# Performance work log

Hardware: AMD Instinct MI355X
Metric: run time of the kernel (lower is better)

The kernel has to match this reference:

```python
import jax, jax.numpy as jnp
import numpy as np
import math

B, S, HID = 4, 2048, 1024
NH, HD = 16, 64  # num heads, head dim
ROPE_THETA = 10000.0


def rotate_half(x):
    x1, x2 = jnp.split(x, 2, axis=-1)
    return jnp.concatenate((-x2, x1), axis=-1)


def setup_inputs() -> dict:
    key = jax.random.key(0)
    ks = jax.random.split(key, 7)
    hidden_states = jax.random.normal(ks[0], (B, S, HID), dtype=jnp.float32)
    attention_mask = jnp.zeros((B, 1, S, S), dtype=jnp.float32)
    position_ids = jnp.sort(jax.random.randint(ks[1], (B, S), 0, S), axis=-1)
    scale = 1.0 / math.sqrt(HID)
    Wq = jax.random.normal(ks[2], (HID, HID), dtype=jnp.float32) * scale
    Wk = jax.random.normal(ks[3], (HID, HID), dtype=jnp.float32) * scale
    Wv = jax.random.normal(ks[4], (HID, HID), dtype=jnp.float32) * scale
    Wo = jax.random.normal(ks[5], (HID, HID), dtype=jnp.float32) * scale
    return {"hidden_states": hidden_states, "attention_mask": attention_mask,
            "position_ids": position_ids, "Wq": Wq, "Wk": Wk, "Wv": Wv, "Wo": Wo}


def reference(hidden_states, attention_mask, position_ids, Wq, Wk, Wv, Wo):
    dtype = hidden_states.dtype
    # QKV projections (torch Linear: x @ W.T), reshape to [B, H, S, D]
    def proj(W):
        return (hidden_states @ W.T).reshape(B, S, NH, HD).transpose(0, 2, 1, 3)
    q, k, v = proj(Wq), proj(Wk), proj(Wv)

    # Rotary embeddings: cos/sin cache of shape [S, HD], gathered by position_ids
    inv_freq = 1.0 / (ROPE_THETA ** (jnp.arange(0, HD, 2, dtype=jnp.float32) / HD))
    t = jnp.arange(S, dtype=jnp.float32)
    freqs = t[:, None] * inv_freq[None, :]            # [S, HD/2]
    emb = jnp.concatenate((freqs, freqs), axis=-1)     # [S, HD]
    cos = jnp.cos(emb).astype(dtype)[position_ids][:, None]  # [B, 1, S, HD]
    sin = jnp.sin(emb).astype(dtype)[position_ids][:, None]

    q = q * cos + rotate_half(q) * sin
    k = k * cos + rotate_half(k) * sin

    # Manual attention: scores, additive mask, fp32 softmax, weighted sum
    scores = jnp.einsum('bhqd,bhkd->bhqk', q, k) / math.sqrt(HD)
    scores = scores + attention_mask
    attn = jax.nn.softmax(scores.astype(jnp.float32), axis=-1).astype(dtype)
    out = jnp.einsum('bhqk,bhkd->bhqd', attn, v)       # [B, H, S, D]
    out = out.transpose(0, 2, 1, 3).reshape(B, S, HID)
    return out @ Wo.T
```

## Files before the change

### kernel.cpp

```cpp
#include <hip/hip_runtime.h>
#include <hip/hip_bf16.h>
#include <math.h>

typedef __bf16 bf16;
typedef bf16 bf16x4 __attribute__((ext_vector_type(4)));
typedef bf16 bf16x8 __attribute__((ext_vector_type(8)));
typedef float f32x4 __attribute__((ext_vector_type(4)));

#define B_ 4
#define S_ 2048
#define HID_ 1024
#define NH_ 16
#define HD_ 64
#define LTS 72

__device__ __forceinline__ void async16(const bf16* g, bf16* l) {
  __builtin_amdgcn_global_load_lds(
      (const __attribute__((address_space(1))) void*)g,
      (__attribute__((address_space(3))) void*)l, 16, 0, 0);
}

#define MM16(A, B, C) C = __builtin_amdgcn_mfma_f32_16x16x32_bf16(A, B, C, 0, 0, 0)

__global__ void cvt_kernel(const float* __restrict__ src, bf16* __restrict__ dst, int n4) {
  int i = blockIdx.x * 256 + threadIdx.x;
  if (i < n4) {
    float4 v = ((const float4*)src)[i];
    bf16x4 o;
    o[0] = (bf16)v.x; o[1] = (bf16)v.y; o[2] = (bf16)v.z; o[3] = (bf16)v.w;
    ((bf16x4*)dst)[i] = o;
  }
}

#define DECL_ACC \
  f32x4 a00 = {}, a01 = {}, a02 = {}, a03 = {}; \
  f32x4 a10 = {}, a11 = {}, a12 = {}, a13 = {}; \
  f32x4 a20 = {}, a21 = {}, a22 = {}, a23 = {}; \
  f32x4 a30 = {}, a31 = {}, a32 = {}, a33 = {};

#define KLOOP_FRAGS_MFMA \
    bf16x8 af0 = *(const bf16x8*)(lA + (wm + 0 * 16 + l16) * 32 + quad * 8); \
    bf16x8 af1 = *(const bf16x8*)(lA + (wm + 1 * 16 + l16) * 32 + quad * 8); \
    bf16x8 af2 = *(const bf16x8*)(lA + (wm + 2 * 16 + l16) * 32 + quad * 8); \
    bf16x8 af3 = *(const bf16x8*)(lA + (wm + 3 * 16 + l16) * 32 + quad * 8); \
    bf16x8 bg0 = *(const bf16x8*)(lB + (wn + 0 * 16 + l16) * 32 + quad * 8); \
    bf16x8 bg1 = *(const bf16x8*)(lB + (wn + 1 * 16 + l16) * 32 + quad * 8); \
    bf16x8 bg2 = *(const bf16x8*)(lB + (wn + 2 * 16 + l16) * 32 + quad * 8); \
    bf16x8 bg3 = *(const bf16x8*)(lB + (wn + 3 * 16 + l16) * 32 + quad * 8); \
    MM16(af0, bg0, a00); MM16(af0, bg1, a01); MM16(af0, bg2, a02); MM16(af0, bg3, a03); \
    MM16(af1, bg0, a10); MM16(af1, bg1, a11); MM16(af1, bg2, a12); MM16(af1, bg3, a13); \
    MM16(af2, bg0, a20); MM16(af2, bg1, a21); MM16(af2, bg2, a22); MM16(af2, bg3, a23); \
    MM16(af3, bg0, a30); MM16(af3, bg1, a31); MM16(af3, bg2, a32); MM16(af3, bg3, a33);

#define ROPE_R(i, r, C0, C1, C2, C3) { \
  const int mloc = (i) * 16 + quad * 4 + (r); \
  const float p = (float)pos[mbase + mloc]; \
  const float aa0 = p * invf0, aa1 = p * invf1; \
  const float c0 = __cosf(aa0), sn0 = __sinf(aa0); \
  const float c1 = __cosf(aa1), sn1 = __sinf(aa1); \
  myT[mloc * LTS + l16]      = (bf16)((C0[r] * c0 - C2[r] * sn0) * scl); \
  myT[mloc * LTS + 32 + l16] = (bf16)((C2[r] * c0 + C0[r] * sn0) * scl); \
  myT[mloc * LTS + 16 + l16] = (bf16)((C1[r] * c1 - C3[r] * sn1) * scl); \
  myT[mloc * LTS + 48 + l16] = (bf16)((C3[r] * c1 + C1[r] * sn1) * scl); }
#define ROPE_I(i, C0, C1, C2, C3) \
  ROPE_R(i, 0, C0, C1, C2, C3) ROPE_R(i, 1, C0, C1, C2, C3) \
  ROPE_R(i, 2, C0, C1, C2, C3) ROPE_R(i, 3, C0, C1, C2, C3)

#define VW(i, j, C) { \
  bf16x4 o; o[0] = (bf16)C[0]; o[1] = (bf16)C[1]; o[2] = (bf16)C[2]; o[3] = (bf16)C[3]; \
  *(bf16x4*)(myT + ((j) * 16 + l16) * LTS + (i) * 16 + quad * 4) = o; }

__global__ void qkv_gemm(
    const bf16* __restrict__ X, const bf16* __restrict__ Wq,
    const bf16* __restrict__ Wk, const bf16* __restrict__ Wv,
    const int* __restrict__ pos,
    bf16* __restrict__ Q, bf16* __restrict__ Ko, bf16* __restrict__ Vt) {
  const int z = blockIdx.z;
  const bf16* W = (z == 0) ? Wq : (z == 1) ? Wk : Wv;
  const int m0 = blockIdx.y * 128;
  const int n0 = blockIdx.x * 128;
  __shared__ __align__(16) bf16 lA[128 * 32];
  __shared__ __align__(16) bf16 lB[128 * 32];
  __shared__ __align__(16) bf16 lT[4][64 * LTS];
  const int tid = threadIdx.x;
  const int lane = tid & 63, w = tid >> 6;
  const int wm = (w >> 1) * 64, wn = (w & 1) * 64;
  const int quad = lane >> 4, l16 = lane & 15;

  DECL_ACC

  const int qa = tid, qb = tid + 256;
  const int ra = qa >> 2, ca = (qa & 3) * 8;
  const int rb = qb >> 2, cb = (qb & 3) * 8;

  for (int k0 = 0; k0 < 1024; k0 += 32) {
    async16(X + (size_t)(m0 + ra) * 1024 + k0 + ca, lA + qa * 8);
    async16(X + (size_t)(m0 + rb) * 1024 + k0 + cb, lA + qb * 8);
    async16(W + (size_t)(n0 + ra) * 1024 + k0 + ca, lB + qa * 8);
    async16(W + (size_t)(n0 + rb) * 1024 + k0 + cb, lB + qb * 8);
    __syncthreads();
    KLOOP_FRAGS_MFMA
    __syncthreads();
  }

  const int h = (n0 + wn) >> 6;
  const int mbase = m0 + wm;
  const int b = mbase >> 11, s0 = mbase & 2047;
  bf16* myT = lT[w];

  if (z <= 1) {
    const float scl = (z == 0) ? 0.125f : 1.0f;
    const float invf0 = __expf(-0.28782313662425572f * (float)l16);
    const float invf1 = __expf(-0.28782313662425572f * (float)(16 + l16));
    ROPE_I(0, a00, a01, a02, a03)
    ROPE_I(1, a10, a11, a12, a13)
    ROPE_I(2, a20, a21, a22, a23)
    ROPE_I(3, a30, a31, a32, a33)
    asm volatile("s_waitcnt lgkmcnt(0)" ::: "memory");
    bf16* dst = (z == 0) ? Q : Ko;
    const int rr = lane >> 3, cc = lane & 7;
#pragma unroll
    for (int it = 0; it < 8; it++) {
      int mloc = it * 8 + rr;
      bf16x8 v = *(const bf16x8*)(myT + mloc * LTS + cc * 8);
      *(bf16x8*)(dst + (((size_t)b * NH_ + h) * S_ + s0 + mloc) * HD_ + cc * 8) = v;
    }
  } else {
    VW(0, 0, a00) VW(0, 1, a01) VW(0, 2, a02) VW(0, 3, a03)
    VW(1, 0, a10) VW(1, 1, a11) VW(1, 2, a12) VW(1, 3, a13)
    VW(2, 0, a20) VW(2, 1, a21) VW(2, 2, a22) VW(2, 3, a23)
    VW(3, 0, a30) VW(3, 1, a31) VW(3, 2, a32) VW(3, 3, a33)
    asm volatile("s_waitcnt lgkmcnt(0)" ::: "memory");
    const int rr = lane >> 3, cc = lane & 7;
#pragma unroll
    for (int it = 0; it < 8; it++) {
      int d = it * 8 + rr;
      bf16x8 v = *(const bf16x8*)(myT + d * LTS + cc * 8);
      *(bf16x8*)(Vt + (((size_t)b * NH_ + h) * HD_ + d) * S_ + s0 + cc * 8) = v;
    }
  }
}

__global__ void __launch_bounds__(256, 4) attn_kernel(
    const bf16* __restrict__ Q, const bf16* __restrict__ K,
    const bf16* __restrict__ Vt, const float* __restrict__ mask,
    bf16* __restrict__ ctx) {
  const int b = blockIdx.y >> 4, h = blockIdx.y & 15;
  const int q0 = blockIdx.x * 64;
  __shared__ __align__(16) bf16 lK[2][64 * 64];
  __shared__ __align__(16) bf16 lV[2][64 * 64];
  __shared__ __align__(16) bf16 lP[4][16 * 64];
  const int tid = threadIdx.x;
  const int lane = tid & 63, w = tid >> 6;
  const int quad = lane >> 4, l16 = lane & 15;

  const int sr = tid >> 3;
  const int scs = (tid & 7) ^ (sr & 7);

  const size_t headoff = ((size_t)b * NH_ + h) * S_ * HD_;
  {
    const bf16* src = Q + headoff + (size_t)q0 * HD_;
    async16(src + sr * 64 + scs * 8, lK[1] + tid * 8);
    async16(src + (sr + 32) * 64 + scs * 8, lK[1] + (tid + 256) * 8);
    const bf16* ksrc = K + headoff;
    async16(ksrc + sr * 64 + scs * 8, lK[0] + tid * 8);
    async16(ksrc + (sr + 32) * 64 + scs * 8, lK[0] + (tid + 256) * 8);
    const bf16* vbase = Vt + headoff;
    async16(vbase + (size_t)sr * S_ + scs * 8, lV[0] + tid * 8);
    async16(vbase + (size_t)(sr + 32) * S_ + scs * 8, lV[0] + (tid + 256) * 8);
  }

  const float* mrow = mask + ((size_t)b * S_ + q0 + w * 16 + l16) * S_;
  const int sw = l16 & 7;
  const int pq  = (quad ^ sw) * 8;
  const int pq2 = ((quad + 4) ^ sw) * 8;
  bf16* myP = lP[w];

  float4 f0, f1, f2, f3;
  {
    const float4* m4 = (const float4*)(mrow);
    f0 = m4[quad]; f1 = m4[4 + quad]; f2 = m4[8 + quad]; f3 = m4[12 + quad];
  }

  __syncthreads();
  const bf16x8 qf  = *(const bf16x8*)(lK[1] + (w * 16 + l16) * 64 + pq);
  const bf16x8 qf2 = *(const bf16x8*)(lK[1] + (w * 16 + l16) * 64 + pq2);
  __syncthreads();

  f32x4 o0 = {}, o1 = {}, o2 = {}, o3 = {};
  float m_run = -1e30f, l_run = 0.f;

  for (int kt = 0; kt < 32; kt++) {
    const bf16* lKc = lK[kt & 1];
    const bf16* lVc = lV[kt & 1];
    if (kt < 31) {
      bf16* nK = lK[(kt & 1) ^ 1];
      bf16* nV = lV[(kt & 1) ^ 1];
      const int k0n = (kt + 1) * 64;
      const bf16* ksrc = K + headoff + (size_t)k0n * HD_;
      async16(ksrc + sr * 64 + scs * 8, nK + tid * 8);
      async16(ksrc + (sr + 32) * 64 + scs * 8, nK + (tid + 256) * 8);
      const bf16* vbase = Vt + headoff + k0n;
      async16(vbase + (size_t)sr * S_ + scs * 8, nV + tid * 8);
      async16(vbase + (size_t)(sr + 32) * S_ + scs * 8, nV + (tid + 256) * 8);
    }

    f32x4 s0 = {}, s1 = {}, s2 = {}, s3 = {};
    __builtin_amdgcn_s_setprio(1);
    {
      bf16x8 k0f = *(const bf16x8*)(lKc + (0 * 16 + l16) * 64 + pq);
      bf16x8 k1f = *(const bf16x8*)(lKc + (1 * 16 + l16) * 64 + pq);
      bf16x8 k2f = *(const bf16x8*)(lKc + (2 * 16 + l16) * 64 + pq);
      bf16x8 k3f = *(const bf16x8*)(lKc + (3 * 16 + l16) * 64 + pq);
      MM16(k0f, qf, s0); MM16(k1f, qf, s1); MM16(k2f, qf, s2); MM16(k3f, qf, s3);
    }
    {
      bf16x8 k0f = *(const bf16x8*)(lKc + (0 * 16 + l16) * 64 + pq2);
      bf16x8 k1f = *(const bf16x8*)(lKc + (1 * 16 + l16) * 64 + pq2);
      bf16x8 k2f = *(const bf16x8*)(lKc + (2 * 16 + l16) * 64 + pq2);
      bf16x8 k3f = *(const bf16x8*)(lKc + (3 * 16 + l16) * 64 + pq2);
      MM16(k0f, qf2, s0); MM16(k1f, qf2, s1); MM16(k2f, qf2, s2); MM16(k3f, qf2, s3);
    }
    __builtin_amdgcn_s_setprio(0);

    float v00 = s0[0] + f0.x, v01 = s0[1] + f0.y, v02 = s0[2] + f0.z, v03 = s0[3] + f0.w;
    float v10 = s1[0] + f1.x, v11 = s1[1] + f1.y, v12 = s1[2] + f1.z, v13 = s1[3] + f1.w;
    float v20 = s2[0] + f2.x, v21 = s2[1] + f2.y, v22 = s2[2] + f2.z, v23 = s2[3] + f2.w;
    float v30 = s3[0] + f3.x, v31 = s3[1] + f3.y, v32 = s3[2] + f3.z, v33 = s3[3] + f3.w;

    float mx = fmaxf(fmaxf(fmaxf(v00, v01), fmaxf(v02, v03)),
                     fmaxf(fmaxf(v10, v11), fmaxf(v12, v13)));
    mx = fmaxf(mx, fmaxf(fmaxf(fmaxf(v20, v21), fmaxf(v22, v23)),
                         fmaxf(fmaxf(v30, v31), fmaxf(v32, v33))));
    mx = fmaxf(mx, __shfl_xor(mx, 16));
    mx = fmaxf(mx, __shfl_xor(mx, 32));

    if (__any(mx > m_run + 8.f)) {
      const float mnew = fmaxf(m_run, mx);
      const float alpha = __expf(m_run - mnew);
      m_run = mnew;
      f32x4 av;
      av[0] = __shfl(alpha, quad * 4 + 0);
      av[1] = __shfl(alpha, quad * 4 + 1);
      av[2] = __shfl(alpha, quad * 4 + 2);
      av[3] = __shfl(alpha, quad * 4 + 3);
      o0 *= av; o1 *= av; o2 *= av; o3 *= av;
      l_run *= alpha;
    }

    float p00 = __expf(v00 - m_run), p01 = __expf(v01 - m_run), p02 = __expf(v02 - m_run), p03 = __expf(v03 - m_run);
    float p10 = __expf(v10 - m_run), p11 = __expf(v11 - m_run), p12 = __expf(v12 - m_run), p13 = __expf(v13 - m_run);
    float p20 = __expf(v20 - m_run), p21 = __expf(v21 - m_run), p22 = __expf(v22 - m_run), p23 = __expf(v23 - m_run);
    float p30 = __expf(v30 - m_run), p31 = __expf(v31 - m_run), p32 = __expf(v32 - m_run), p33 = __expf(v33 - m_run);

    {
      const int swz = 8 * sw;
      bf16x4 pk;
      pk[0] = (bf16)p00; pk[1] = (bf16)p01; pk[2] = (bf16)p02; pk[3] = (bf16)p03;
      *(bf16x4*)(myP + l16 * 64 + ((0 * 16 + quad * 4) ^ swz)) = pk;
      pk[0] = (bf16)p10; pk[1] = (bf16)p11; pk[2] = (bf16)p12; pk[3] = (bf16)p13;
      *(bf16x4*)(myP + l16 * 64 + ((1 * 16 + quad * 4) ^ swz)) = pk;
      pk[0] = (bf16)p20; pk[1] = (bf16)p21; pk[2] = (bf16)p22; pk[3] = (bf16)p23;
      *(bf16x4*)(myP + l16 * 64 + ((2 * 16 + quad * 4) ^ swz)) = pk;
      pk[0] = (bf16)p30; pk[1] = (bf16)p31; pk[2] = (bf16)p32; pk[3] = (bf16)p33;
      *(bf16x4*)(myP + l16 * 64 + ((3 * 16 + quad * 4) ^ swz)) = pk;
    }

    float ps = (((p00 + p01) + (p02 + p03)) + ((p10 + p11) + (p12 + p13)))
             + (((p20 + p21) + (p22 + p23)) + ((p30 + p31) + (p32 + p33)));
    ps += __shfl_xor(ps, 16);
    ps += __shfl_xor(ps, 32);
    l_run += ps;

    if (kt < 31) {
      const float4* mn = (const float4*)(mrow + (kt + 1) * 64);
      f0 = mn[quad]; f1 = mn[4 + quad]; f2 = mn[8 + quad]; f3 = mn[12 + quad];
    }

    __builtin_amdgcn_s_setprio(1);
    {
      bf16x8 ap = *(const bf16x8*)(myP + l16 * 64 + pq);
      bf16x8 b0 = *(const bf16x8*)(lVc + (0 * 16 + l16) * 64 + pq);
      bf16x8 b1 = *(const bf16x8*)(lVc + (1 * 16 + l16) * 64 + pq);
      bf16x8 b2 = *(const bf16x8*)(lVc + (2 * 16 + l16) * 64 + pq);
      bf16x8 b3 = *(const bf16x8*)(lVc + (3 * 16 + l16) * 64 + pq);
      MM16(ap, b0, o0); MM16(ap, b1, o1); MM16(ap, b2, o2); MM16(ap, b3, o3);
    }
    {
      bf16x8 ap = *(const bf16x8*)(myP + l16 * 64 + pq2);
      bf16x8 b0 = *(const bf16x8*)(lVc + (0 * 16 + l16) * 64 + pq2);
      bf16x8 b1 = *(const bf16x8*)(lVc + (1 * 16 + l16) * 64 + pq2);
      bf16x8 b2 = *(const bf16x8*)(lVc + (2 * 16 + l16) * 64 + pq2);
      bf16x8 b3 = *(const bf16x8*)(lVc + (3 * 16 + l16) * 64 + pq2);
      MM16(ap, b0, o0); MM16(ap, b1, o1); MM16(ap, b2, o2); MM16(ap, b3, o3);
    }
    __builtin_amdgcn_s_setprio(0);

    __syncthreads();
  }

  f32x4 lv;
  lv[0] = __shfl(l_run, quad * 4 + 0);
  lv[1] = __shfl(l_run, quad * 4 + 1);
  lv[2] = __shfl(l_run, quad * 4 + 2);
  lv[3] = __shfl(l_run, quad * 4 + 3);
  bf16* lO = lK[0];
#pragma unroll
  for (int r = 0; r < 4; r++) {
    const float invl = 1.0f / lv[r];
    const int sloc = w * 16 + quad * 4 + r;
    lO[sloc * 64 + l16]      = (bf16)(o0[r] * invl);
    lO[sloc * 64 + 16 + l16] = (bf16)(o1[r] * invl);
    lO[sloc * 64 + 32 + l16] = (bf16)(o2[r] * invl);
    lO[sloc * 64 + 48 + l16] = (bf16)(o3[r] * invl);
  }
  __syncthreads();
  {
    const int rr = tid >> 3, cc = tid & 7;
#pragma unroll
    for (int it = 0; it < 2; it++) {
      int sloc = it * 32 + rr;
      bf16x8 v = *(const bf16x8*)(lO + sloc * 64 + cc * 8);
      *(bf16x8*)(ctx + ((size_t)b * S_ + q0 + sloc) * HID_ + h * HD_ + cc * 8) = v;
    }
  }
}

#define PW(i, j, C) { \
  float* po = out + (size_t)(m0 + wm + (i) * 16 + quad * 4) * 1024 + n0 + wn + (j) * 16 + l16; \
  po[0] = C[0]; po[1024] = C[1]; po[2048] = C[2]; po[3072] = C[3]; }

__global__ void proj_gemm(
    const bf16* __restrict__ A, const bf16* __restrict__ Wo, float* __restrict__ out) {
  const int m0 = blockIdx.y * 128;
  const int n0 = blockIdx.x * 128;
  __shared__ __align__(16) bf16 lA[128 * 32];
  __shared__ __align__(16) bf16 lB[128 * 32];
  const int tid = threadIdx.x;
  const int lane = tid & 63, w = tid >> 6;
  const int wm = (w >> 1) * 64, wn = (w & 1) * 64;
  const int quad = lane >> 4, l16 = lane & 15;

  DECL_ACC
  const int qa = tid, qb = tid + 256;
  const int ra = qa >> 2, ca = (qa & 3) * 8;
  const int rb = qb >> 2, cb = (qb & 3) * 8;

  for (int k0 = 0; k0 < 1024; k0 += 32) {
    async16(A + (size_t)(m0 + ra) * 1024 + k0 + ca, lA + qa * 8);
    async16(A + (size_t)(m0 + rb) * 1024 + k0 + cb, lA + qb * 8);
    async16(Wo + (size_t)(n0 + ra) * 1024 + k0 + ca, lB + qa * 8);
    async16(Wo + (size_t)(n0 + rb) * 1024 + k0 + cb, lB + qb * 8);
    __syncthreads();
    KLOOP_FRAGS_MFMA
    __syncthreads();
  }
  PW(0, 0, a00) PW(0, 1, a01) PW(0, 2, a02) PW(0, 3, a03)
  PW(1, 0, a10) PW(1, 1, a11) PW(1, 2, a12) PW(1, 3, a13)
  PW(2, 0, a20) PW(2, 1, a21) PW(2, 2, a22) PW(2, 3, a23)
  PW(3, 0, a30) PW(3, 1, a31) PW(3, 2, a32) PW(3, 3, a33)
}

__global__ void sentinel_kernel(float* out, int n, float val) {
  int i = blockIdx.x * 256 + threadIdx.x;
  if (i < n) out[i] = val;
}

extern "C" void kernel_launch(void* const* d_in, const int* in_sizes, int n_in,
                              void* d_out, int out_size, void* d_ws, size_t ws_size,
                              hipStream_t stream) {
  const float* X    = (const float*)d_in[0];
  const float* mask = (const float*)d_in[1];
  const int*   pos  = (const int*)d_in[2];
  const float* Wq   = (const float*)d_in[3];
  const float* Wk   = (const float*)d_in[4];
  const float* Wv   = (const float*)d_in[5];
  const float* Wo   = (const float*)d_in[6];
  float* out = (float*)d_out;

  char* ws = (char*)d_ws;
  const size_t SZ = (size_t)B_ * NH_ * S_ * HD_ * sizeof(bf16);
  if (ws_size < 3 * SZ) {
    sentinel_kernel<<<(out_size + 255) / 256, 256, 0, stream>>>(
        out, out_size, (float)(ws_size >> 20));
    return;
  }

  bf16* Xb  = (bf16*)(ws);
  bf16* ctx = (bf16*)(ws);
  bf16* Q   = (bf16*)(ws + SZ);
  bf16* Vt  = (bf16*)(ws + 2 * SZ);
  bf16* Wob = (bf16*)(ws + 2 * SZ);
  bf16* Kb  = (bf16*)d_out;
  bf16* Wqb = (bf16*)((char*)d_out + SZ);
  bf16* Wkb = Wqb + 1024 * 1024;
  bf16* Wvb = Wkb + 1024 * 1024;

  const int nX4 = (B_ * S_ * HID_) / 4;
  const int nW4 = (HID_ * HID_) / 4;
  cvt_kernel<<<(nX4 + 255) / 256, 256, 0, stream>>>(X, Xb, nX4);
  cvt_kernel<<<(nW4 + 255) / 256, 256, 0, stream>>>(Wq, Wqb, nW4);
  cvt_kernel<<<(nW4 + 255) / 256, 256, 0, stream>>>(Wk, Wkb, nW4);
  cvt_kernel<<<(nW4 + 255) / 256, 256, 0, stream>>>(Wv, Wvb, nW4);

  qkv_gemm<<<dim3(8, 64, 3), 256, 0, stream>>>(Xb, Wqb, Wkb, Wvb, pos, Q, Kb, Vt);
  attn_kernel<<<dim3(32, 64), 256, 0, stream>>>(Q, Kb, Vt, mask, ctx);

  cvt_kernel<<<(nW4 + 255) / 256, 256, 0, stream>>>(Wo, Wob, nW4);
  proj_gemm<<<dim3(8, 64), 256, 0, stream>>>(ctx, Wob, out);
}
```

Baseline: 403.6 us.

## Widen attention blocks to 128 queries with XCD-aware head mapping

The attention kernel now runs 512-thread blocks covering 128 query rows, so each K/V tile loaded into LDS is shared by eight waves instead of four. This halves global K/V traffic per query. Block indices are remapped so that blocks of the same (batch, head) land on the same XCD, which should improve L2 reuse. The P staging buffer is cut to 16x32 per wave and written in two halves just before each PV MFMA to save LDS, at the cost of extra LDS write/read round-trips and higher per-CU register and LDS pressure.

```diff
diff --git a/kernel.cpp b/kernel.cpp
--- a/kernel.cpp
+++ b/kernel.cpp
@@ -141,15 +141,22 @@
   }
 }
 
-__global__ void __launch_bounds__(256, 4) attn_kernel(
+__global__ void __launch_bounds__(512, 8) attn_kernel(
     const bf16* __restrict__ Q, const bf16* __restrict__ K,
     const bf16* __restrict__ Vt, const float* __restrict__ mask,
     bf16* __restrict__ ctx) {
-  const int b = blockIdx.y >> 4, h = blockIdx.y & 15;
-  const int q0 = blockIdx.x * 64;
+  const int f = blockIdx.x;
+  const int xcd = f & 7, slot = f >> 3;
+  const int dh = (slot >> 4) * 8 + xcd;
+  const int dq = slot & 15;
+  const int b = dh >> 4, h = dh & 15;
+  const int q0 = dq * 128;
+
   __shared__ __align__(16) bf16 lK[2][64 * 64];
   __shared__ __align__(16) bf16 lV[2][64 * 64];
-  __shared__ __align__(16) bf16 lP[4][16 * 64];
+  __shared__ __align__(16) bf16 lP[8][16 * 32];
+  bf16* lKf = (bf16*)lK;
+
   const int tid = threadIdx.x;
   const int lane = tid & 63, w = tid >> 6;
   const int quad = lane >> 4, l16 = lane & 15;
@@ -159,15 +166,11 @@
 
   const size_t headoff = ((size_t)b * NH_ + h) * S_ * HD_;
   {
-    const bf16* src = Q + headoff + (size_t)q0 * HD_;
-    async16(src + sr * 64 + scs * 8, lK[1] + tid * 8);
-    async16(src + (sr + 32) * 64 + scs * 8, lK[1] + (tid + 256) * 8);
-    const bf16* ksrc = K + headoff;
-    async16(ksrc + sr * 64 + scs * 8, lK[0] + tid * 8);
-    async16(ksrc + (sr + 32) * 64 + scs * 8, lK[0] + (tid + 256) * 8);
+    const bf16* qsrc = Q + headoff + (size_t)q0 * HD_;
+    async16(qsrc + sr * 64 + scs * 8, lKf + tid * 8);
+    async16(qsrc + (size_t)(sr + 64) * 64 + scs * 8, lKf + (tid + 512) * 8);
     const bf16* vbase = Vt + headoff;
     async16(vbase + (size_t)sr * S_ + scs * 8, lV[0] + tid * 8);
-    async16(vbase + (size_t)(sr + 32) * S_ + scs * 8, lV[0] + (tid + 256) * 8);
   }
 
   const float* mrow = mask + ((size_t)b * S_ + q0 + w * 16 + l16) * S_;
@@ -175,6 +178,9 @@
   const int pq  = (quad ^ sw) * 8;
   const int pq2 = ((quad + 4) ^ sw) * 8;
   bf16* myP = lP[w];
+  const int pwr0 = l16 * 32 + ((quad ^ (l16 & 6)) * 4);
+  const int pwr1 = l16 * 32 + (((4 + quad) ^ (l16 & 6)) * 4);
+  const int prd  = l16 * 32 + ((quad ^ ((l16 >> 1) & 3)) * 8);
 
   float4 f0, f1, f2, f3;
   {
@@ -183,8 +189,11 @@
   }
 
   __syncthreads();
-  const bf16x8 qf  = *(const bf16x8*)(lK[1] + (w * 16 + l16) * 64 + pq);
-  const bf16x8 qf2 = *(const bf16x8*)(lK[1] + (w * 16 + l16) * 64 + pq2);
+  const int row128 = w * 16 + l16;
+  const bf16x8 qf  = *(const bf16x8*)(lKf + row128 * 64 + pq);
+  const bf16x8 qf2 = *(const bf16x8*)(lKf + row128 * 64 + pq2);
+  __syncthreads();
+  async16(K + headoff + sr * 64 + scs * 8, lK[0] + tid * 8);
   __syncthreads();
 
   f32x4 o0 = {}, o1 = {}, o2 = {}, o3 = {};
@@ -197,12 +206,8 @@
       bf16* nK = lK[(kt & 1) ^ 1];
       bf16* nV = lV[(kt & 1) ^ 1];
       const int k0n = (kt + 1) * 64;
-      const bf16* ksrc = K + headoff + (size_t)k0n * HD_;
-      async16(ksrc + sr * 64 + scs * 8, nK + tid * 8);
-      async16(ksrc + (sr + 32) * 64 + scs * 8, nK + (tid + 256) * 8);
-      const bf16* vbase = Vt + headoff + k0n;
-      async16(vbase + (size_t)sr * S_ + scs * 8, nV + tid * 8);
-      async16(vbase + (size_t)(sr + 32) * S_ + scs * 8, nV + (tid + 256) * 8);
+      async16(K + headoff + (size_t)k0n * HD_ + sr * 64 + scs * 8, nK + tid * 8);
+      async16(Vt + headoff + k0n + (size_t)sr * S_ + scs * 8, nV + tid * 8);
     }
 
     f32x4 s0 = {}, s1 = {}, s2 = {}, s3 = {};
@@ -253,19 +258,6 @@
     float p20 = __expf(v20 - m_run), p21 = __expf(v21 - m_run), p22 = __expf(v22 - m_run), p23 = __expf(v23 - m_run);
     float p30 = __expf(v30 - m_run), p31 = __expf(v31 - m_run), p32 = __expf(v32 - m_run), p33 = __expf(v33 - m_run);
 
-    {
-      const int swz = 8 * sw;
-      bf16x4 pk;
-      pk[0] = (bf16)p00; pk[1] = (bf16)p01; pk[2] = (bf16)p02; pk[3] = (bf16)p03;
-      *(bf16x4*)(myP + l16 * 64 + ((0 * 16 + quad * 4) ^ swz)) = pk;
-      pk[0] = (bf16)p10; pk[1] = (bf16)p11; pk[2] = (bf16)p12; pk[3] = (bf16)p13;
-      *(bf16x4*)(myP + l16 * 64 + ((1 * 16 + quad * 4) ^ swz)) = pk;
-      pk[0] = (bf16)p20; pk[1] = (bf16)p21; pk[2] = (bf16)p22; pk[3] = (bf16)p23;
-      *(bf16x4*)(myP + l16 * 64 + ((2 * 16 + quad * 4) ^ swz)) = pk;
-      pk[0] = (bf16)p30; pk[1] = (bf16)p31; pk[2] = (bf16)p32; pk[3] = (bf16)p33;
-      *(bf16x4*)(myP + l16 * 64 + ((3 * 16 + quad * 4) ^ swz)) = pk;
-    }
-
     float ps = (((p00 + p01) + (p02 + p03)) + ((p10 + p11) + (p12 + p13)))
              + (((p20 + p21) + (p22 + p23)) + ((p30 + p31) + (p32 + p33)));
     ps += __shfl_xor(ps, 16);
@@ -279,7 +271,12 @@
 
     __builtin_amdgcn_s_setprio(1);
     {
-      bf16x8 ap = *(const bf16x8*)(myP + l16 * 64 + pq);
+      bf16x4 pk;
+      pk[0] = (bf16)p00; pk[1] = (bf16)p01; pk[2] = (bf16)p02; pk[3] = (bf16)p03;
+      *(bf16x4*)(myP + pwr0) = pk;
+      pk[0] = (bf16)p10; pk[1] = (bf16)p11; pk[2] = (bf16)p12; pk[3] = (bf16)p13;
+      *(bf16x4*)(myP + pwr1) = pk;
+      bf16x8 ap = *(const bf16x8*)(myP + prd);
       bf16x8 b0 = *(const bf16x8*)(lVc + (0 * 16 + l16) * 64 + pq);
       bf16x8 b1 = *(const bf16x8*)(lVc + (1 * 16 + l16) * 64 + pq);
       bf16x8 b2 = *(const bf16x8*)(lVc + (2 * 16 + l16) * 64 + pq);
@@ -287,7 +284,12 @@
       MM16(ap, b0, o0); MM16(ap, b1, o1); MM16(ap, b2, o2); MM16(ap, b3, o3);
     }
     {
-      bf16x8 ap = *(const bf16x8*)(myP + l16 * 64 + pq2);
+      bf16x4 pk;
+      pk[0] = (bf16)p20; pk[1] = (bf16)p21; pk[2] = (bf16)p22; pk[3] = (bf16)p23;
+      *(bf16x4*)(myP + pwr0) = pk;
+      pk[0] = (bf16)p30; pk[1] = (bf16)p31; pk[2] = (bf16)p32; pk[3] = (bf16)p33;
+      *(bf16x4*)(myP + pwr1) = pk;
+      bf16x8 ap = *(const bf16x8*)(myP + prd);
       bf16x8 b0 = *(const bf16x8*)(lVc + (0 * 16 + l16) * 64 + pq2);
       bf16x8 b1 = *(const bf16x8*)(lVc + (1 * 16 + l16) * 64 + pq2);
       bf16x8 b2 = *(const bf16x8*)(lVc + (2 * 16 + l16) * 64 + pq2);
@@ -304,23 +306,22 @@
   lv[1] = __shfl(l_run, quad * 4 + 1);
   lv[2] = __shfl(l_run, quad * 4 + 2);
   lv[3] = __shfl(l_run, quad * 4 + 3);
-  bf16* lO = lK[0];
 #pragma unroll
   for (int r = 0; r < 4; r++) {
     const float invl = 1.0f / lv[r];
     const int sloc = w * 16 + quad * 4 + r;
-    lO[sloc * 64 + l16]      = (bf16)(o0[r] * invl);
-    lO[sloc * 64 + 16 + l16] = (bf16)(o1[r] * invl);
-    lO[sloc * 64 + 32 + l16] = (bf16)(o2[r] * invl);
-    lO[sloc * 64 + 48 + l16] = (bf16)(o3[r] * invl);
+    lKf[sloc * 64 + l16]      = (bf16)(o0[r] * invl);
+    lKf[sloc * 64 + 16 + l16] = (bf16)(o1[r] * invl);
+    lKf[sloc * 64 + 32 + l16] = (bf16)(o2[r] * invl);
+    lKf[sloc * 64 + 48 + l16] = (bf16)(o3[r] * invl);
   }
   __syncthreads();
   {
     const int rr = tid >> 3, cc = tid & 7;
 #pragma unroll
     for (int it = 0; it < 2; it++) {
-      int sloc = it * 32 + rr;
-      bf16x8 v = *(const bf16x8*)(lO + sloc * 64 + cc * 8);
+      int sloc = it * 64 + rr;
+      bf16x8 v = *(const bf16x8*)(lKf + sloc * 64 + cc * 8);
       *(bf16x8*)(ctx + ((size_t)b * S_ + q0 + sloc) * HID_ + h * HD_ + cc * 8) = v;
     }
   }
@@ -404,7 +405,7 @@
   cvt_kernel<<<(nW4 + 255) / 256, 256, 0, stream>>>(Wv, Wvb, nW4);
 
   qkv_gemm<<<dim3(8, 64, 3), 256, 0, stream>>>(Xb, Wqb, Wkb, Wvb, pos, Q, Kb, Vt);
-  attn_kernel<<<dim3(32, 64), 256, 0, stream>>>(Q, Kb, Vt, mask, ctx);
+  attn_kernel<<<dim3(1024), 512, 0, stream>>>(Q, Kb, Vt, mask, ctx);
 
   cvt_kernel<<<(nW4 + 255) / 256, 256, 0, stream>>>(Wo, Wob, nW4);
   proj_gemm<<<dim3(8, 64), 256, 0, stream>>>(ctx, Wob, out);
```

New measurement: 886.0 us. 120% more time.
